# Kernel tuning notes

Hardware: AMD Instinct MI355X
Metric: run time of the kernel (lower is better)

Reference implementation:

```python
import jax, jax.numpy as jnp
import numpy as np

S, B, K = 1024, 16, 1024
QD, KD = 1024, 1024


def setup_inputs() -> dict:
    key = jax.random.key(0)
    k1, k2, k3, k4 = jax.random.split(key, 4)
    queries = jax.random.normal(k1, (S, B, QD), dtype=jnp.float32)
    keys = jax.random.normal(k2, (B, K, KD), dtype=jnp.float32)
    null_mask = jax.random.randint(k3, (B, K), 0, 2).astype(jnp.bool_)
    W_in = jax.random.normal(k4, (KD, QD), dtype=jnp.float32) * 0.02
    return {"queries": queries, "keys": keys, "null_mask": null_mask, "W_in": W_in}


def reference(queries, keys, null_mask, W_in):
    # queries: (S, B, QD); keys: (B, K, KD); null_mask: (B, K); W_in: (KD, QD)
    t_query = jnp.einsum('sbq,dq->sbd', queries, W_in)          # linear_in, no bias
    alpha = jnp.einsum('sbd,bkd->sbk', t_query, keys)           # unscaled bilinear scores
    alpha = jnp.where(null_mask[None, :, :], -jnp.inf, alpha)   # masked_fill_
    att_weight = jax.nn.softmax(alpha, axis=2)                  # (S, B, K)
    attened_keys = jnp.einsum('sbk,bkd->sbd', att_weight, keys) # (S, B, KD)
    return (attened_keys, alpha)
```

## Files before the change

### kernel.cpp

```cpp
#include <hip/hip_runtime.h>
#include <math.h>

#define S_DIM 1024
#define B_DIM 16
#define K_DIM 1024
#define QD_DIM 1024
#define KD_DIM 1024
#define MASK_NEG (-3.0e38f)

using short4v = __attribute__((ext_vector_type(4))) short;
using short8v = __attribute__((ext_vector_type(8))) short;
using float4v = __attribute__((ext_vector_type(4))) float;

constexpr int TILE = 128;
constexpr int BK   = 32;
constexpr int LDK  = 36;

#define MFMA(a, b, c) __builtin_amdgcn_mfma_f32_16x16x32_bf16(a, b, c, 0, 0, 0)

__device__ inline void split4(const float4 v, uint2& hi, uint2& lo) {
    uint ax = __float_as_uint(v.x), ay = __float_as_uint(v.y);
    uint az = __float_as_uint(v.z), aw = __float_as_uint(v.w);
    hi.x = __builtin_amdgcn_perm(ay, ax, 0x07060302u);
    hi.y = __builtin_amdgcn_perm(aw, az, 0x07060302u);
    float rx = v.x - __uint_as_float(ax & 0xFFFF0000u);
    float ry = v.y - __uint_as_float(ay & 0xFFFF0000u);
    float rz = v.z - __uint_as_float(az & 0xFFFF0000u);
    float rw = v.w - __uint_as_float(aw & 0xFFFF0000u);
    lo.x = __builtin_amdgcn_perm(__float_as_uint(ry), __float_as_uint(rx), 0x07060302u);
    lo.y = __builtin_amdgcn_perm(__float_as_uint(rw), __float_as_uint(rz), 0x07060302u);
}

__device__ inline short8v frag_load(const short* base) {
    short4v a = *(const short4v*)base;
    short4v b = *(const short4v*)(base + 4);
    return __builtin_shufflevector(a, b, 0, 1, 2, 3, 4, 5, 6, 7);
}

__global__ __launch_bounds__(256) void g1_mfma(const float* __restrict__ Q,
                                               const float* __restrict__ W,
                                               float* __restrict__ TQ) {
    __shared__ short Ah[TILE * LDK], Al[TILE * LDK], Bh[TILE * LDK], Bl[TILE * LDK];
    const int t = threadIdx.x;
    const int lane = t & 63, w = t >> 6;
    const int wm = w >> 1, wn = w & 1;
    const int quad = lane >> 4, l15 = lane & 15;
    const int m0 = blockIdx.y * TILE, n0 = blockIdx.x * TILE;
    const int sr = t >> 3;
    const int sc = (t & 7) * 4;

    float4v acc[4][4] = {};

    for (int k0 = 0; k0 < QD_DIM; k0 += BK) {
        #pragma unroll
        for (int i = 0; i < 4; ++i) {
            const int r = sr + i * 32;
            uint2 h, l;
            float4 va = *(const float4*)(Q + (size_t)(m0 + r) * QD_DIM + k0 + sc);
            split4(va, h, l);
            *(uint2*)&Ah[r * LDK + sc] = h;
            *(uint2*)&Al[r * LDK + sc] = l;
            float4 vb = *(const float4*)(W + (size_t)(n0 + r) * QD_DIM + k0 + sc);
            split4(vb, h, l);
            *(uint2*)&Bh[r * LDK + sc] = h;
            *(uint2*)&Bl[r * LDK + sc] = l;
        }
        __syncthreads();
        short8v ah[4], al[4];
        #pragma unroll
        for (int mt = 0; mt < 4; ++mt) {
            const int ar = (wm * 64 + mt * 16 + l15) * LDK + quad * 8;
            ah[mt] = frag_load(&Ah[ar]);
            al[mt] = frag_load(&Al[ar]);
        }
        #pragma unroll
        for (int nt = 0; nt < 4; ++nt) {
            const int br = (wn * 64 + nt * 16 + l15) * LDK + quad * 8;
            short8v bh = frag_load(&Bh[br]);
            short8v bl = frag_load(&Bl[br]);
            #pragma unroll
            for (int mt = 0; mt < 4; ++mt) acc[mt][nt] = MFMA(ah[mt], bh, acc[mt][nt]);
            #pragma unroll
            for (int mt = 0; mt < 4; ++mt) acc[mt][nt] = MFMA(al[mt], bh, acc[mt][nt]);
            #pragma unroll
            for (int mt = 0; mt < 4; ++mt) acc[mt][nt] = MFMA(ah[mt], bl, acc[mt][nt]);
        }
        __syncthreads();
    }
    #pragma unroll
    for (int mt = 0; mt < 4; ++mt)
        #pragma unroll
        for (int reg = 0; reg < 4; ++reg) {
            const int m = m0 + wm * 64 + mt * 16 + quad * 4 + reg;
            #pragma unroll
            for (int nt = 0; nt < 4; ++nt) {
                const int n = n0 + wn * 64 + nt * 16 + l15;
                TQ[(size_t)m * KD_DIM + n] = acc[mt][nt][reg];
            }
        }
}

__global__ __launch_bounds__(256) void g2_mfma(const float* __restrict__ TQ,
                                               const float* __restrict__ keys,
                                               const int* __restrict__ mask,
                                               float* __restrict__ alpha) {
    __shared__ short Ah[TILE * LDK], Al[TILE * LDK], Bh[TILE * LDK], Bl[TILE * LDK];
    const int t = threadIdx.x;
    const int lane = t & 63, w = t >> 6;
    const int wm = w >> 1, wn = w & 1;
    const int quad = lane >> 4, l15 = lane & 15;
    const int m0 = blockIdx.y * TILE, n0 = blockIdx.x * TILE;
    const int b = blockIdx.z;
    const int sr = t >> 3;
    const int sc = (t & 7) * 4;

    const float* Kb = keys + (size_t)b * K_DIM * KD_DIM;

    float4v acc[4][4] = {};

    for (int k0 = 0; k0 < KD_DIM; k0 += BK) {
        #pragma unroll
        for (int i = 0; i < 4; ++i) {
            const int r = sr + i * 32;
            uint2 h, l;
            float4 va = *(const float4*)(TQ + ((size_t)(m0 + r) * B_DIM + b) * QD_DIM + k0 + sc);
            split4(va, h, l);
            *(uint2*)&Ah[r * LDK + sc] = h;
            *(uint2*)&Al[r * LDK + sc] = l;
            float4 vb = *(const float4*)(Kb + (size_t)(n0 + r) * KD_DIM + k0 + sc);
            split4(vb, h, l);
            *(uint2*)&Bh[r * LDK + sc] = h;
            *(uint2*)&Bl[r * LDK + sc] = l;
        }
        __syncthreads();
        short8v ah[4], al[4];
        #pragma unroll
        for (int mt = 0; mt < 4; ++mt) {
            const int ar = (wm * 64 + mt * 16 + l15) * LDK + quad * 8;
            ah[mt] = frag_load(&Ah[ar]);
            al[mt] = frag_load(&Al[ar]);
        }
        #pragma unroll
        for (int nt = 0; nt < 4; ++nt) {
            const int br = (wn * 64 + nt * 16 + l15) * LDK + quad * 8;
            short8v bh = frag_load(&Bh[br]);
            short8v bl = frag_load(&Bl[br]);
            #pragma unroll
            for (int mt = 0; mt < 4; ++mt) acc[mt][nt] = MFMA(ah[mt], bh, acc[mt][nt]);
            #pragma unroll
            for (int mt = 0; mt < 4; ++mt) acc[mt][nt] = MFMA(al[mt], bh, acc[mt][nt]);
            #pragma unroll
            for (int mt = 0; mt < 4; ++mt) acc[mt][nt] = MFMA(ah[mt], bl, acc[mt][nt]);
        }
        __syncthreads();
    }
    int mk[4];
    #pragma unroll
    for (int nt = 0; nt < 4; ++nt)
        mk[nt] = mask[b * K_DIM + n0 + wn * 64 + nt * 16 + l15];
    #pragma unroll
    for (int mt = 0; mt < 4; ++mt)
        #pragma unroll
        for (int reg = 0; reg < 4; ++reg) {
            const int m = m0 + wm * 64 + mt * 16 + quad * 4 + reg;
            #pragma unroll
            for (int nt = 0; nt < 4; ++nt) {
                const int n = n0 + wn * 64 + nt * 16 + l15;
                alpha[((size_t)m * B_DIM + b) * K_DIM + n] = mk[nt] ? MASK_NEG : acc[mt][nt][reg];
            }
        }
}

__global__ __launch_bounds__(256) void k_stats(const float* __restrict__ alpha,
                                               float* __restrict__ mx,
                                               float* __restrict__ il) {
    const int r = blockIdx.x;
    const int t = threadIdx.x;
    const float4 v = ((const float4*)(alpha + (size_t)r * K_DIM))[t];
    float m = fmaxf(fmaxf(v.x, v.y), fmaxf(v.z, v.w));
    #pragma unroll
    for (int o = 1; o < 64; o <<= 1) m = fmaxf(m, __shfl_xor(m, o, 64));
    __shared__ float redm[4];
    __shared__ float reds[4];
    const int wid = t >> 6;
    if ((t & 63) == 0) redm[wid] = m;
    __syncthreads();
    const float M = fmaxf(fmaxf(redm[0], redm[1]), fmaxf(redm[2], redm[3]));
    float s = expf(v.x - M) + expf(v.y - M) + expf(v.z - M) + expf(v.w - M);
    #pragma unroll
    for (int o = 1; o < 64; o <<= 1) s += __shfl_xor(s, o, 64);
    if ((t & 63) == 0) reds[wid] = s;
    __syncthreads();
    if (t == 0) {
        mx[r] = M;
        il[r] = 1.0f / (reds[0] + reds[1] + reds[2] + reds[3]);
    }
}

__global__ __launch_bounds__(256) void g3_mfma(const float* __restrict__ alpha,
                                               const float* __restrict__ keys,
                                               const float* __restrict__ mx,
                                               const float* __restrict__ il,
                                               float* __restrict__ outk) {
    __shared__ short Ah[TILE * LDK], Al[TILE * LDK], Bh[TILE * LDK], Bl[TILE * LDK];
    __shared__ float Ms[TILE], Ls[TILE];
    const int t = threadIdx.x;
    const int lane = t & 63, w = t >> 6;
    const int wm = w >> 1, wn = w & 1;
    const int quad = lane >> 4, l15 = lane & 15;
    const int m0 = blockIdx.y * TILE, n0 = blockIdx.x * TILE;
    const int b = blockIdx.z;
    const int sr = t >> 3;
    const int sc = (t & 7) * 4;

    const float* Kb = keys + (size_t)b * K_DIM * KD_DIM;

    if (t < TILE) {
        Ms[t] = mx[(size_t)(m0 + t) * B_DIM + b];
        Ls[t] = il[(size_t)(m0 + t) * B_DIM + b];
    }
    __syncthreads();

    float4v acc[4][4] = {};

    for (int k0 = 0; k0 < K_DIM; k0 += BK) {
        #pragma unroll
        for (int i = 0; i < 4; ++i) {
            const int r = sr + i * 32;
            float4 va = *(const float4*)(alpha + ((size_t)(m0 + r) * B_DIM + b) * K_DIM + k0 + sc);
            const float Mv = Ms[r], Lv = Ls[r];
            float4 p;
            p.x = __expf(va.x - Mv) * Lv;
            p.y = __expf(va.y - Mv) * Lv;
            p.z = __expf(va.z - Mv) * Lv;
            p.w = __expf(va.w - Mv) * Lv;
            uint2 h, l;
            split4(p, h, l);
            *(uint2*)&Ah[r * LDK + sc] = h;
            *(uint2*)&Al[r * LDK + sc] = l;
        }
        {
            const int kb = (t >> 5) * 4;
            const int dc = (t & 31) * 4;
            float4 f[4];
            #pragma unroll
            for (int i = 0; i < 4; ++i)
                f[i] = *(const float4*)(Kb + (size_t)(k0 + kb + i) * KD_DIM + n0 + dc);
            #pragma unroll
            for (int e = 0; e < 4; ++e) {
                float4 g;
                g.x = (&f[0].x)[e]; g.y = (&f[1].x)[e];
                g.z = (&f[2].x)[e]; g.w = (&f[3].x)[e];
                uint2 h, l;
                split4(g, h, l);
                *(uint2*)&Bh[(dc + e) * LDK + kb] = h;
                *(uint2*)&Bl[(dc + e) * LDK + kb] = l;
            }
        }
        __syncthreads();
        short8v ah[4], al[4];
        #pragma unroll
        for (int mt = 0; mt < 4; ++mt) {
            const int ar = (wm * 64 + mt * 16 + l15) * LDK + quad * 8;
            ah[mt] = frag_load(&Ah[ar]);
            al[mt] = frag_load(&Al[ar]);
        }
        #pragma unroll
        for (int nt = 0; nt < 4; ++nt) {
            const int br = (wn * 64 + nt * 16 + l15) * LDK + quad * 8;
            short8v bh = frag_load(&Bh[br]);
            short8v bl = frag_load(&Bl[br]);
            #pragma unroll
            for (int mt = 0; mt < 4; ++mt) acc[mt][nt] = MFMA(ah[mt], bh, acc[mt][nt]);
            #pragma unroll
            for (int mt = 0; mt < 4; ++mt) acc[mt][nt] = MFMA(al[mt], bh, acc[mt][nt]);
            #pragma unroll
            for (int mt = 0; mt < 4; ++mt) acc[mt][nt] = MFMA(ah[mt], bl, acc[mt][nt]);
        }
        __syncthreads();
    }
    #pragma unroll
    for (int mt = 0; mt < 4; ++mt)
        #pragma unroll
        for (int reg = 0; reg < 4; ++reg) {
            const int m = m0 + wm * 64 + mt * 16 + quad * 4 + reg;
            #pragma unroll
            for (int nt = 0; nt < 4; ++nt) {
                const int n = n0 + wn * 64 + nt * 16 + l15;
                outk[((size_t)m * B_DIM + b) * KD_DIM + n] = acc[mt][nt][reg];
            }
        }
}

extern "C" void kernel_launch(void* const* d_in, const int* in_sizes, int n_in,
                              void* d_out, int out_size, void* d_ws, size_t ws_size,
                              hipStream_t stream) {
    const float* queries = (const float*)d_in[0];
    const float* keys    = (const float*)d_in[1];
    const int*   mask    = (const int*)d_in[2];
    const float* W_in    = (const float*)d_in[3];

    float* out_attened = (float*)d_out;
    float* out_alpha   = (float*)d_out + (size_t)S_DIM * B_DIM * KD_DIM;

    float* tq = (float*)d_ws;
    float* mx = tq + (size_t)S_DIM * B_DIM * QD_DIM;
    float* il = mx + (size_t)S_DIM * B_DIM;

    dim3 blk(256);

    dim3 grid1(KD_DIM / TILE, (S_DIM * B_DIM) / TILE);
    g1_mfma<<<grid1, blk, 0, stream>>>(queries, W_in, tq);

    dim3 grid2(K_DIM / TILE, S_DIM / TILE, B_DIM);
    g2_mfma<<<grid2, blk, 0, stream>>>(tq, keys, mask, out_alpha);

    k_stats<<<dim3(S_DIM * B_DIM), blk, 0, stream>>>(out_alpha, mx, il);

    dim3 grid3(KD_DIM / TILE, S_DIM / TILE, B_DIM);
    g3_mfma<<<grid3, blk, 0, stream>>>(out_alpha, keys, mx, il, out_attened);
}
```

Before: 605.6 us.

## Pre-split operands into bf16 hi/lo arrays and stream them via global_load_lds

Adds pre-pass kernels that split queries and keys into bf16 hi/lo halves, plus a transposed split of keys for the final GEMM. The GEMMs then load those halves straight into LDS with global_load_lds instead of splitting fp32 tiles in registers on every reload. The first GEMM now writes the projected queries as split bf16 through an LDS-staged epilogue. This trades repeated per-tile split work and fp32 traffic for extra pre-pass kernels and workspace reuse (output buffers serve as scratch), and it relies on unpadded 32-wide LDS rows.

```diff
diff --git a/kernel.cpp b/kernel.cpp
--- a/kernel.cpp
+++ b/kernel.cpp
@@ -8,19 +8,22 @@
 #define KD_DIM 1024
 #define MASK_NEG (-3.0e38f)
 
+typedef unsigned short u16;
+typedef unsigned int u32;
 using short4v = __attribute__((ext_vector_type(4))) short;
 using short8v = __attribute__((ext_vector_type(8))) short;
 using float4v = __attribute__((ext_vector_type(4))) float;
 
-constexpr int TILE = 128;
-constexpr int BK   = 32;
-constexpr int LDK  = 36;
-
 #define MFMA(a, b, c) __builtin_amdgcn_mfma_f32_16x16x32_bf16(a, b, c, 0, 0, 0)
 
+__device__ __forceinline__ void load_lds16(const void* g, void* l) {
+    __builtin_amdgcn_global_load_lds((const __attribute__((address_space(1))) u32*)g,
+                                     (__attribute__((address_space(3))) u32*)l, 16, 0, 0);
+}
+
 __device__ inline void split4(const float4 v, uint2& hi, uint2& lo) {
-    uint ax = __float_as_uint(v.x), ay = __float_as_uint(v.y);
-    uint az = __float_as_uint(v.z), aw = __float_as_uint(v.w);
+    u32 ax = __float_as_uint(v.x), ay = __float_as_uint(v.y);
+    u32 az = __float_as_uint(v.z), aw = __float_as_uint(v.w);
     hi.x = __builtin_amdgcn_perm(ay, ax, 0x07060302u);
     hi.y = __builtin_amdgcn_perm(aw, az, 0x07060302u);
     float rx = v.x - __uint_as_float(ax & 0xFFFF0000u);
@@ -31,53 +34,110 @@
     lo.y = __builtin_amdgcn_perm(__float_as_uint(rw), __float_as_uint(rz), 0x07060302u);
 }
 
+__device__ __forceinline__ u16 hi16(float f) { return (u16)(__float_as_uint(f) >> 16); }
+__device__ __forceinline__ u16 lo16(float f) {
+    float r = f - __uint_as_float(__float_as_uint(f) & 0xFFFF0000u);
+    return (u16)(__float_as_uint(r) >> 16);
+}
+
 __device__ inline short8v frag_load(const short* base) {
     short4v a = *(const short4v*)base;
     short4v b = *(const short4v*)(base + 4);
     return __builtin_shufflevector(a, b, 0, 1, 2, 3, 4, 5, 6, 7);
 }
 
-__global__ __launch_bounds__(256) void g1_mfma(const float* __restrict__ Q,
+__global__ __launch_bounds__(256) void k_split(const float* __restrict__ in,
+                                               u16* __restrict__ H, u16* __restrict__ L) {
+    const size_t i = (size_t)blockIdx.x * 256 + threadIdx.x;
+    float4 v = ((const float4*)in)[i];
+    uint2 h, l;
+    split4(v, h, l);
+    ((uint2*)H)[i] = h;
+    ((uint2*)L)[i] = l;
+}
+
+__global__ __launch_bounds__(256) void k_tsplit(const float* __restrict__ keys,
+                                                u16* __restrict__ TH, u16* __restrict__ TL) {
+    __shared__ float tile[64][65];
+    const int b = blockIdx.z, k0 = blockIdx.x * 64, d0 = blockIdx.y * 64;
+    const float* Kb = keys + (size_t)b * K_DIM * KD_DIM;
+    const int t = threadIdx.x;
+    const int rk = t >> 4;
+    const int cd = (t & 15) * 4;
+    #pragma unroll
+    for (int i = 0; i < 4; ++i) {
+        float4 v = *(const float4*)(Kb + (size_t)(k0 + rk + i * 16) * KD_DIM + d0 + cd);
+        tile[cd + 0][rk + i * 16] = v.x;
+        tile[cd + 1][rk + i * 16] = v.y;
+        tile[cd + 2][rk + i * 16] = v.z;
+        tile[cd + 3][rk + i * 16] = v.w;
+    }
+    __syncthreads();
+    const int rd = t >> 4;
+    const int ck = (t & 15) * 4;
+    #pragma unroll
+    for (int i = 0; i < 4; ++i) {
+        const int d = rd + i * 16;
+        float4 g;
+        g.x = tile[d][ck + 0]; g.y = tile[d][ck + 1];
+        g.z = tile[d][ck + 2]; g.w = tile[d][ck + 3];
+        uint2 h, l;
+        split4(g, h, l);
+        const size_t off = (size_t)b * KD_DIM * K_DIM + (size_t)(d0 + d) * K_DIM + k0 + ck;
+        *(uint2*)(TH + off) = h;
+        *(uint2*)(TL + off) = l;
+    }
+}
+
+__global__ __launch_bounds__(256) void g1_mfma(const u16* __restrict__ Qh,
+                                               const u16* __restrict__ Ql,
                                                const float* __restrict__ W,
-                                               float* __restrict__ TQ) {
-    __shared__ short Ah[TILE * LDK], Al[TILE * LDK], Bh[TILE * LDK], Bl[TILE * LDK];
-    const int t = threadIdx.x;
-    const int lane = t & 63, w = t >> 6;
-    const int wm = w >> 1, wn = w & 1;
-    const int quad = lane >> 4, l15 = lane & 15;
-    const int m0 = blockIdx.y * TILE, n0 = blockIdx.x * TILE;
-    const int sr = t >> 3;
-    const int sc = (t & 7) * 4;
+                                               u16* __restrict__ TQh,
+                                               u16* __restrict__ TQl) {
+    __shared__ short LDS[17408];
+    short* Ah = LDS;
+    short* Al = LDS + 4096;
+    short* Bh = LDS + 8192;
+    short* Bl = LDS + 12800;
+    const int t = threadIdx.x, w = t >> 6, l = t & 63;
+    const int wm = w >> 1, wn = w & 1, quad = l >> 4, l15 = l & 15;
+    const int m0 = blockIdx.y * 128, n0 = blockIdx.x * 128;
+    const int arow = w * 16 + (l >> 2);
+    const int achk = (l & 3) * 8;
+    const int brr = t >> 3;
+    const int bcc = (t & 7) * 4;
 
     float4v acc[4][4] = {};
 
-    for (int k0 = 0; k0 < QD_DIM; k0 += BK) {
+    for (int k0 = 0; k0 < QD_DIM; k0 += 32) {
+        #pragma unroll
+        for (int r = 0; r < 2; ++r) {
+            const size_t goff = (size_t)(m0 + r * 64 + arow) * QD_DIM + k0 + achk;
+            load_lds16(Qh + goff, Ah + (r * 64 + w * 16) * 32);
+            load_lds16(Ql + goff, Al + (r * 64 + w * 16) * 32);
+        }
         #pragma unroll
         for (int i = 0; i < 4; ++i) {
-            const int r = sr + i * 32;
-            uint2 h, l;
-            float4 va = *(const float4*)(Q + (size_t)(m0 + r) * QD_DIM + k0 + sc);
-            split4(va, h, l);
-            *(uint2*)&Ah[r * LDK + sc] = h;
-            *(uint2*)&Al[r * LDK + sc] = l;
-            float4 vb = *(const float4*)(W + (size_t)(n0 + r) * QD_DIM + k0 + sc);
-            split4(vb, h, l);
-            *(uint2*)&Bh[r * LDK + sc] = h;
-            *(uint2*)&Bl[r * LDK + sc] = l;
+            const int r = brr + i * 32;
+            float4 v = *(const float4*)(W + (size_t)(n0 + r) * QD_DIM + k0 + bcc);
+            uint2 h, lo;
+            split4(v, h, lo);
+            *(uint2*)&Bh[r * 36 + bcc] = h;
+            *(uint2*)&Bl[r * 36 + bcc] = lo;
         }
         __syncthreads();
         short8v ah[4], al[4];
         #pragma unroll
         for (int mt = 0; mt < 4; ++mt) {
-            const int ar = (wm * 64 + mt * 16 + l15) * LDK + quad * 8;
-            ah[mt] = frag_load(&Ah[ar]);
-            al[mt] = frag_load(&Al[ar]);
+            const int ar = (wm * 64 + mt * 16 + l15) * 32 + quad * 8;
+            ah[mt] = *(const short8v*)&Ah[ar];
+            al[mt] = *(const short8v*)&Al[ar];
         }
         #pragma unroll
         for (int nt = 0; nt < 4; ++nt) {
-            const int br = (wn * 64 + nt * 16 + l15) * LDK + quad * 8;
-            short8v bh = frag_load(&Bh[br]);
-            short8v bl = frag_load(&Bl[br]);
+            const int br2 = (wn * 64 + nt * 16 + l15) * 36 + quad * 8;
+            short8v bh = frag_load(&Bh[br2]);
+            short8v bl = frag_load(&Bl[br2]);
             #pragma unroll
             for (int mt = 0; mt < 4; ++mt) acc[mt][nt] = MFMA(ah[mt], bh, acc[mt][nt]);
             #pragma unroll
@@ -87,86 +147,111 @@
         }
         __syncthreads();
     }
+    short* C16 = LDS;
+    const int erow = t >> 1, ecol = (t & 1) * 64;
     #pragma unroll
     for (int mt = 0; mt < 4; ++mt)
         #pragma unroll
         for (int reg = 0; reg < 4; ++reg) {
-            const int m = m0 + wm * 64 + mt * 16 + quad * 4 + reg;
+            const int ml = wm * 64 + mt * 16 + quad * 4 + reg;
+            #pragma unroll
+            for (int nt = 0; nt < 4; ++nt)
+                C16[ml * 128 + wn * 64 + nt * 16 + l15] = (short)hi16(acc[mt][nt][reg]);
+        }
+    __syncthreads();
+    #pragma unroll
+    for (int i = 0; i < 8; ++i) {
+        const int jj = ((i + (t & 7)) & 7) * 8;
+        *(short8v*)(TQh + (size_t)(m0 + erow) * KD_DIM + n0 + ecol + jj) =
+            *(const short8v*)&C16[erow * 128 + ecol + jj];
+    }
+    __syncthreads();
+    #pragma unroll
+    for (int mt = 0; mt < 4; ++mt)
+        #pragma unroll
+        for (int reg = 0; reg < 4; ++reg) {
+            const int ml = wm * 64 + mt * 16 + quad * 4 + reg;
+            #pragma unroll
+            for (int nt = 0; nt < 4; ++nt)
+                C16[ml * 128 + wn * 64 + nt * 16 + l15] = (short)lo16(acc[mt][nt][reg]);
+        }
+    __syncthreads();
+    #pragma unroll
+    for (int i = 0; i < 8; ++i) {
+        const int jj = ((i + (t & 7)) & 7) * 8;
+        *(short8v*)(TQl + (size_t)(m0 + erow) * KD_DIM + n0 + ecol + jj) =
+            *(const short8v*)&C16[erow * 128 + ecol + jj];
+    }
+}
+
+__global__ __launch_bounds__(256) void g2_mfma(const u16* __restrict__ TQh,
+                                               const u16* __restrict__ TQl,
+                                               const u16* __restrict__ KH,
+                                               const u16* __restrict__ KL,
+                                               const int* __restrict__ mask,
+                                               float* __restrict__ alpha) {
+    __shared__ short LDS[16384];
+    short* Ah = LDS;
+    short* Al = LDS + 4096;
+    short* Bh = LDS + 8192;
+    short* Bl = LDS + 12288;
+    const int t = threadIdx.x, w = t >> 6, l = t & 63;
+    const int wm = w >> 1, wn = w & 1, quad = l >> 4, l15 = l & 15;
+    const int m0 = blockIdx.y * 128, n0 = blockIdx.x * 128;
+    const int b = blockIdx.z;
+    const int arow = w * 16 + (l >> 2);
+    const int achk = (l & 3) * 8;
+
+    const u16* KHb = KH + (size_t)b * K_DIM * KD_DIM;
+    const u16* KLb = KL + (size_t)b * K_DIM * KD_DIM;
+
+    float4v acc[4][4] = {};
+
+    for (int k0 = 0; k0 < KD_DIM; k0 += 32) {
+        #pragma unroll
+        for (int r = 0; r < 2; ++r) {
+            const size_t aoff = ((size_t)(m0 + r * 64 + arow) * B_DIM + b) * QD_DIM + k0 + achk;
+            load_lds16(TQh + aoff, Ah + (r * 64 + w * 16) * 32);
+            load_lds16(TQl + aoff, Al + (r * 64 + w * 16) * 32);
+            const size_t boff = (size_t)(n0 + r * 64 + arow) * KD_DIM + k0 + achk;
+            load_lds16(KHb + boff, Bh + (r * 64 + w * 16) * 32);
+            load_lds16(KLb + boff, Bl + (r * 64 + w * 16) * 32);
+        }
+        __syncthreads();
+        short8v ah[4], al[4];
+        #pragma unroll
+        for (int mt = 0; mt < 4; ++mt) {
+            const int ar = (wm * 64 + mt * 16 + l15) * 32 + quad * 8;
+            ah[mt] = *(const short8v*)&Ah[ar];
+            al[mt] = *(const short8v*)&Al[ar];
+        }
+        #pragma unroll
+        for (int nt = 0; nt < 4; ++nt) {
+            const int br2 = (wn * 64 + nt * 16 + l15) * 32 + quad * 8;
+            short8v bh = *(const short8v*)&Bh[br2];
+            short8v bl = *(const short8v*)&Bl[br2];
+            #pragma unroll
+            for (int mt = 0; mt < 4; ++mt) acc[mt][nt] = MFMA(ah[mt], bh, acc[mt][nt]);
+            #pragma unroll
+            for (int mt = 0; mt < 4; ++mt) acc[mt][nt] = MFMA(al[mt], bh, acc[mt][nt]);
+            #pragma unroll
+            for (int mt = 0; mt < 4; ++mt) acc[mt][nt] = MFMA(ah[mt], bl, acc[mt][nt]);
+        }
+        __syncthreads();
+    }
+    int mk[4];
+    #pragma unroll
+    for (int nt = 0; nt < 4; ++nt)
+        mk[nt] = mask[b * K_DIM + n0 + wn * 64 + nt * 16 + l15];
+    #pragma unroll
+    for (int mt = 0; mt < 4; ++mt)
+        #pragma unroll
+        for (int reg = 0; reg < 4; ++reg) {
+            const int s = m0 + wm * 64 + mt * 16 + quad * 4 + reg;
             #pragma unroll
             for (int nt = 0; nt < 4; ++nt) {
                 const int n = n0 + wn * 64 + nt * 16 + l15;
-                TQ[(size_t)m * KD_DIM + n] = acc[mt][nt][reg];
-            }
-        }
-}
-
-__global__ __launch_bounds__(256) void g2_mfma(const float* __restrict__ TQ,
-                                               const float* __restrict__ keys,
-                                               const int* __restrict__ mask,
-                                               float* __restrict__ alpha) {
-    __shared__ short Ah[TILE * LDK], Al[TILE * LDK], Bh[TILE * LDK], Bl[TILE * LDK];
-    const int t = threadIdx.x;
-    const int lane = t & 63, w = t >> 6;
-    const int wm = w >> 1, wn = w & 1;
-    const int quad = lane >> 4, l15 = lane & 15;
-    const int m0 = blockIdx.y * TILE, n0 = blockIdx.x * TILE;
-    const int b = blockIdx.z;
-    const int sr = t >> 3;
-    const int sc = (t & 7) * 4;
-
-    const float* Kb = keys + (size_t)b * K_DIM * KD_DIM;
-
-    float4v acc[4][4] = {};
-
-    for (int k0 = 0; k0 < KD_DIM; k0 += BK) {
-        #pragma unroll
-        for (int i = 0; i < 4; ++i) {
-            const int r = sr + i * 32;
-            uint2 h, l;
-            float4 va = *(const float4*)(TQ + ((size_t)(m0 + r) * B_DIM + b) * QD_DIM + k0 + sc);
-            split4(va, h, l);
-            *(uint2*)&Ah[r * LDK + sc] = h;
-            *(uint2*)&Al[r * LDK + sc] = l;
-            float4 vb = *(const float4*)(Kb + (size_t)(n0 + r) * KD_DIM + k0 + sc);
-            split4(vb, h, l);
-            *(uint2*)&Bh[r * LDK + sc] = h;
-            *(uint2*)&Bl[r * LDK + sc] = l;
-        }
-        __syncthreads();
-        short8v ah[4], al[4];
-        #pragma unroll
-        for (int mt = 0; mt < 4; ++mt) {
-            const int ar = (wm * 64 + mt * 16 + l15) * LDK + quad * 8;
-            ah[mt] = frag_load(&Ah[ar]);
-            al[mt] = frag_load(&Al[ar]);
-        }
-        #pragma unroll
-        for (int nt = 0; nt < 4; ++nt) {
-            const int br = (wn * 64 + nt * 16 + l15) * LDK + quad * 8;
-            short8v bh = frag_load(&Bh[br]);
-            short8v bl = frag_load(&Bl[br]);
-            #pragma unroll
-            for (int mt = 0; mt < 4; ++mt) acc[mt][nt] = MFMA(ah[mt], bh, acc[mt][nt]);
-            #pragma unroll
-            for (int mt = 0; mt < 4; ++mt) acc[mt][nt] = MFMA(al[mt], bh, acc[mt][nt]);
-            #pragma unroll
-            for (int mt = 0; mt < 4; ++mt) acc[mt][nt] = MFMA(ah[mt], bl, acc[mt][nt]);
-        }
-        __syncthreads();
-    }
-    int mk[4];
-    #pragma unroll
-    for (int nt = 0; nt < 4; ++nt)
-        mk[nt] = mask[b * K_DIM + n0 + wn * 64 + nt * 16 + l15];
-    #pragma unroll
-    for (int mt = 0; mt < 4; ++mt)
-        #pragma unroll
-        for (int reg = 0; reg < 4; ++reg) {
-            const int m = m0 + wm * 64 + mt * 16 + quad * 4 + reg;
-            #pragma unroll
-            for (int nt = 0; nt < 4; ++nt) {
-                const int n = n0 + wn * 64 + nt * 16 + l15;
-                alpha[((size_t)m * B_DIM + b) * K_DIM + n] = mk[nt] ? MASK_NEG : acc[mt][nt][reg];
+                alpha[((size_t)s * B_DIM + b) * K_DIM + n] = mk[nt] ? MASK_NEG : acc[mt][nt][reg];
             }
         }
 }
@@ -198,24 +283,30 @@
 }
 
 __global__ __launch_bounds__(256) void g3_mfma(const float* __restrict__ alpha,
-                                               const float* __restrict__ keys,
+                                               const u16* __restrict__ TH,
+                                               const u16* __restrict__ TL,
                                                const float* __restrict__ mx,
                                                const float* __restrict__ il,
                                                float* __restrict__ outk) {
-    __shared__ short Ah[TILE * LDK], Al[TILE * LDK], Bh[TILE * LDK], Bl[TILE * LDK];
-    __shared__ float Ms[TILE], Ls[TILE];
-    const int t = threadIdx.x;
-    const int lane = t & 63, w = t >> 6;
-    const int wm = w >> 1, wn = w & 1;
-    const int quad = lane >> 4, l15 = lane & 15;
-    const int m0 = blockIdx.y * TILE, n0 = blockIdx.x * TILE;
+    __shared__ short LDS[17408];
+    __shared__ float Ms[128], Ls[128];
+    short* Ah = LDS;
+    short* Al = LDS + 4608;
+    short* Bh = LDS + 9216;
+    short* Bl = LDS + 13312;
+    const int t = threadIdx.x, w = t >> 6, l = t & 63;
+    const int wm = w >> 1, wn = w & 1, quad = l >> 4, l15 = l & 15;
+    const int m0 = blockIdx.y * 128, n0 = blockIdx.x * 128;
     const int b = blockIdx.z;
-    const int sr = t >> 3;
-    const int sc = (t & 7) * 4;
-
-    const float* Kb = keys + (size_t)b * K_DIM * KD_DIM;
-
-    if (t < TILE) {
+    const int arow = w * 16 + (l >> 2);
+    const int achk = (l & 3) * 8;
+    const int prr = t >> 3;
+    const int pcc = (t & 7) * 4;
+
+    const u16* THb = TH + (size_t)b * KD_DIM * K_DIM;
+    const u16* TLb = TL + (size_t)b * KD_DIM * K_DIM;
+
+    if (t < 128) {
         Ms[t] = mx[(size_t)(m0 + t) * B_DIM + b];
         Ls[t] = il[(size_t)(m0 + t) * B_DIM + b];
     }
@@ -223,53 +314,41 @@
 
     float4v acc[4][4] = {};
 
-    for (int k0 = 0; k0 < K_DIM; k0 += BK) {
+    for (int k0 = 0; k0 < K_DIM; k0 += 32) {
+        #pragma unroll
+        for (int r = 0; r < 2; ++r) {
+            const size_t boff = (size_t)(n0 + r * 64 + arow) * K_DIM + k0 + achk;
+            load_lds16(THb + boff, Bh + (r * 64 + w * 16) * 32);
+            load_lds16(TLb + boff, Bl + (r * 64 + w * 16) * 32);
+        }
         #pragma unroll
         for (int i = 0; i < 4; ++i) {
-            const int r = sr + i * 32;
-            float4 va = *(const float4*)(alpha + ((size_t)(m0 + r) * B_DIM + b) * K_DIM + k0 + sc);
+            const int r = prr + i * 32;
+            float4 va = *(const float4*)(alpha + ((size_t)(m0 + r) * B_DIM + b) * K_DIM + k0 + pcc);
             const float Mv = Ms[r], Lv = Ls[r];
             float4 p;
             p.x = __expf(va.x - Mv) * Lv;
             p.y = __expf(va.y - Mv) * Lv;
             p.z = __expf(va.z - Mv) * Lv;
             p.w = __expf(va.w - Mv) * Lv;
-            uint2 h, l;
-            split4(p, h, l);
-            *(uint2*)&Ah[r * LDK + sc] = h;
-            *(uint2*)&Al[r * LDK + sc] = l;
-        }
-        {
-            const int kb = (t >> 5) * 4;
-            const int dc = (t & 31) * 4;
-            float4 f[4];
-            #pragma unroll
-            for (int i = 0; i < 4; ++i)
-                f[i] = *(const float4*)(Kb + (size_t)(k0 + kb + i) * KD_DIM + n0 + dc);
-            #pragma unroll
-            for (int e = 0; e < 4; ++e) {
-                float4 g;
-                g.x = (&f[0].x)[e]; g.y = (&f[1].x)[e];
-                g.z = (&f[2].x)[e]; g.w = (&f[3].x)[e];
-                uint2 h, l;
-                split4(g, h, l);
-                *(uint2*)&Bh[(dc + e) * LDK + kb] = h;
-                *(uint2*)&Bl[(dc + e) * LDK + kb] = l;
-            }
+            uint2 h, lo;
+            split4(p, h, lo);
+            *(uint2*)&Ah[r * 36 + pcc] = h;
+            *(uint2*)&Al[r * 36 + pcc] = lo;
         }
         __syncthreads();
         short8v ah[4], al[4];
         #pragma unroll
         for (int mt = 0; mt < 4; ++mt) {
-            const int ar = (wm * 64 + mt * 16 + l15) * LDK + quad * 8;
+            const int ar = (wm * 64 + mt * 16 + l15) * 36 + quad * 8;
             ah[mt] = frag_load(&Ah[ar]);
             al[mt] = frag_load(&Al[ar]);
         }
         #pragma unroll
         for (int nt = 0; nt < 4; ++nt) {
-            const int br = (wn * 64 + nt * 16 + l15) * LDK + quad * 8;
-            short8v bh = frag_load(&Bh[br]);
-            short8v bl = frag_load(&Bl[br]);
+            const int br2 = (wn * 64 + nt * 16 + l15) * 32 + quad * 8;
+            short8v bh = *(const short8v*)&Bh[br2];
+            short8v bl = *(const short8v*)&Bl[br2];
             #pragma unroll
             for (int mt = 0; mt < 4; ++mt) acc[mt][nt] = MFMA(ah[mt], bh, acc[mt][nt]);
             #pragma unroll
@@ -283,11 +362,11 @@
     for (int mt = 0; mt < 4; ++mt)
         #pragma unroll
         for (int reg = 0; reg < 4; ++reg) {
-            const int m = m0 + wm * 64 + mt * 16 + quad * 4 + reg;
+            const int s = m0 + wm * 64 + mt * 16 + quad * 4 + reg;
             #pragma unroll
             for (int nt = 0; nt < 4; ++nt) {
                 const int n = n0 + wn * 64 + nt * 16 + l15;
-                outk[((size_t)m * B_DIM + b) * KD_DIM + n] = acc[mt][nt][reg];
+                outk[((size_t)s * B_DIM + b) * KD_DIM + n] = acc[mt][nt][reg];
             }
         }
 }
@@ -300,23 +379,38 @@
     const int*   mask    = (const int*)d_in[2];
     const float* W_in    = (const float*)d_in[3];
 
-    float* out_attened = (float*)d_out;
-    float* out_alpha   = (float*)d_out + (size_t)S_DIM * B_DIM * KD_DIM;
-
-    float* tq = (float*)d_ws;
-    float* mx = tq + (size_t)S_DIM * B_DIM * QD_DIM;
-    float* il = mx + (size_t)S_DIM * B_DIM;
+    const size_t NM = (size_t)S_DIM * B_DIM * QD_DIM;
+
+    float* out_att   = (float*)d_out;
+    float* out_alpha = (float*)d_out + NM;
+
+    u16* keysH  = (u16*)d_ws;
+    u16* keysL  = keysH + NM;
+    u16* keysTH = keysH;
+    u16* keysTL = keysL;
+    float* mx = (float*)(keysL + NM);
+    float* il = mx + S_DIM * B_DIM;
+
+    u16* Qh = (u16*)out_alpha;
+    u16* Ql = Qh + NM;
+    u16* TQh = (u16*)out_att;
+    u16* TQl = TQh + NM;
 
     dim3 blk(256);
 
-    dim3 grid1(KD_DIM / TILE, (S_DIM * B_DIM) / TILE);
-    g1_mfma<<<grid1, blk, 0, stream>>>(queries, W_in, tq);
-
-    dim3 grid2(K_DIM / TILE, S_DIM / TILE, B_DIM);
-    g2_mfma<<<grid2, blk, 0, stream>>>(tq, keys, mask, out_alpha);
+    k_split<<<dim3(16384), blk, 0, stream>>>(queries, Qh, Ql);
+    k_split<<<dim3(16384), blk, 0, stream>>>(keys, keysH, keysL);
+
+    dim3 grid1(KD_DIM / 128, (S_DIM * B_DIM) / 128);
+    g1_mfma<<<grid1, blk, 0, stream>>>(Qh, Ql, W_in, TQh, TQl);
+
+    dim3 grid2(K_DIM / 128, S_DIM / 128, B_DIM);
+    g2_mfma<<<grid2, blk, 0, stream>>>(TQh, TQl, keysH, keysL, mask, out_alpha);
 
     k_stats<<<dim3(S_DIM * B_DIM), blk, 0, stream>>>(out_alpha, mx, il);
 
-    dim3 grid3(KD_DIM / TILE, S_DIM / TILE, B_DIM);
-    g3_mfma<<<grid3, blk, 0, stream>>>(out_alpha, keys, mx, il, out_attened);
-}
+    k_tsplit<<<dim3(16, 16, 16), blk, 0, stream>>>(keys, keysTH, keysTL);
+
+    dim3 grid3(KD_DIM / 128, S_DIM / 128, B_DIM);
+    g3_mfma<<<grid3, blk, 0, stream>>>(out_alpha, keysTH, keysTL, mx, il, out_att);
+}
```

Measured after the change: 670.2 us. 10.7% more time.
